# Kernel tuning notes

Hardware: AMD Instinct MI355X
Metric: run time of the kernel (lower is better)

The kernel has to match this reference:

```python
import jax, jax.numpy as jnp
import numpy as np

B, T, D = 64, 1024, 512

def setup_inputs() -> dict:
    key = jax.random.key(0)
    ks = jax.random.split(key, 5)
    s_in = 1.0 / np.sqrt(2 * D)
    s_m = 1.0 / np.sqrt(D)
    return {
        "x": jax.random.normal(ks[0], (B, T, D), dtype=jnp.float32),
        "tau_w": jax.random.normal(ks[1], (D, 2 * D), dtype=jnp.float32) * s_in,
        "tau_b": jax.random.normal(ks[2], (D,), dtype=jnp.float32) * s_in,
        "mem_w": jax.random.normal(ks[3], (D, D), dtype=jnp.float32) * s_m,
        "mem_b": jax.random.normal(ks[4], (D,), dtype=jnp.float32) * s_m,
        "threshold": jnp.asarray(0.5, dtype=jnp.float32),
    }

def reference(x, tau_w, tau_b, mem_w, mem_b, threshold):
    b, t, d = x.shape
    dt = x.dtype
    # tau_fc input is cat([xt, tau]); split weight into x-part and tau-part
    Wx = tau_w[:, :d]   # [D, D] acting on xt
    Wt = tau_w[:, d:]   # [D, D] acting on previous tau
    # precompute the parts that depend only on x (dropout=0 -> identity)
    xproj = jnp.einsum('btd,ed->bte', x, Wx) + tau_b      # tau_fc x-contribution
    m = jnp.einsum('btd,ed->bte', x, mem_w) + mem_b       # mem_fc(xt)

    def step(carry, inp):
        v, tau = carry
        xp_t, m_t = inp
        tau = jax.nn.sigmoid(xp_t + tau @ Wt.T)
        alpha = jnp.exp(-1.0 / (tau + 1e-6))
        v = alpha * v + (1.0 - alpha) * m_t
        s = (v >= threshold).astype(dt)
        v = v * (1.0 - s)
        return (v, tau), s

    v0 = jnp.zeros((b, d), dtype=dt)
    tau0 = jnp.ones((b, d), dtype=dt)
    (v, tau), spikes = jax.lax.scan(
        step, (v0, tau0),
        (jnp.swapaxes(xproj, 0, 1), jnp.swapaxes(m, 0, 1)))
    return jnp.swapaxes(spikes, 0, 1), tau, v
```

## Files before the change

kernel.cpp:

```cpp
#include <hip/hip_runtime.h>

#define BB 64
#define TT 1024
#define DD 512
#define BT (BB*TT)

#define TAUG_SLOTS (2ULL * 64 * 4 * 3 * 128)
#define SENT32 0xFFFFFFFFu

typedef float f4 __attribute__((ext_vector_type(4)));

__global__ __launch_bounds__(256, 2) void gemm_kernel(
    const float* __restrict__ x, const float* __restrict__ tau_w,
    const float* __restrict__ tau_b, const float* __restrict__ mem_w,
    const float* __restrict__ mem_b, float* __restrict__ xp, float* __restrict__ mm)
{
    __shared__ float As[32][132];
    __shared__ float Bs[32][68];

    const int tid  = threadIdx.x;
    const int bt0  = blockIdx.x * 128;
    const bool isxp = (blockIdx.y < 8);
    const float* W       = isxp ? tau_w : mem_w;
    const int    wstride = isxp ? 1024 : 512;
    const int    e0      = isxp ? blockIdx.y * 64 : blockIdx.y * 64 - 512;
    const float* bias    = isxp ? tau_b : mem_b;
    float*       dst     = isxp ? xp : mm;

    const int tm = tid & 31, tn = tid >> 5;
    const int lr = tid >> 3, lc = tid & 7;

    float bias_r[8];
#pragma unroll
    for (int ni = 0; ni < 8; ni++) bias_r[ni] = bias[e0 + tn * 8 + ni];

    float acc[4][8] = {};
    float4 pa[4], pb[2];

#pragma unroll
    for (int j = 0; j < 4; j++)
        pa[j] = *(const float4*)(x + (size_t)(bt0 + lr + 32 * j) * DD + lc * 4);
#pragma unroll
    for (int j = 0; j < 2; j++)
        pb[j] = *(const float4*)(W + (size_t)(e0 + lr + 32 * j) * wstride + lc * 4);

    for (int kb = 0; kb < DD; kb += 32) {
#pragma unroll
        for (int j = 0; j < 4; j++) {
            As[lc * 4 + 0][lr + 32 * j] = pa[j].x;
            As[lc * 4 + 1][lr + 32 * j] = pa[j].y;
            As[lc * 4 + 2][lr + 32 * j] = pa[j].z;
            As[lc * 4 + 3][lr + 32 * j] = pa[j].w;
        }
#pragma unroll
        for (int j = 0; j < 2; j++) {
            Bs[lc * 4 + 0][lr + 32 * j] = pb[j].x;
            Bs[lc * 4 + 1][lr + 32 * j] = pb[j].y;
            Bs[lc * 4 + 2][lr + 32 * j] = pb[j].z;
            Bs[lc * 4 + 3][lr + 32 * j] = pb[j].w;
        }
        __syncthreads();
        if (kb + 32 < DD) {
#pragma unroll
            for (int j = 0; j < 4; j++)
                pa[j] = *(const float4*)(x + (size_t)(bt0 + lr + 32 * j) * DD + kb + 32 + lc * 4);
#pragma unroll
            for (int j = 0; j < 2; j++)
                pb[j] = *(const float4*)(W + (size_t)(e0 + lr + 32 * j) * wstride + kb + 32 + lc * 4);
        }
#pragma unroll
        for (int k = 0; k < 32; k++) {
            float4 av  = *(const float4*)&As[k][tm * 4];
            float4 bv0 = *(const float4*)&Bs[k][tn * 8];
            float4 bv1 = *(const float4*)&Bs[k][tn * 8 + 4];
            float a_[4] = {av.x, av.y, av.z, av.w};
            float b_[8] = {bv0.x, bv0.y, bv0.z, bv0.w, bv1.x, bv1.y, bv1.z, bv1.w};
#pragma unroll
            for (int mi = 0; mi < 4; mi++)
#pragma unroll
                for (int ni = 0; ni < 8; ni++)
                    acc[mi][ni] = fmaf(a_[mi], b_[ni], acc[mi][ni]);
        }
        __syncthreads();
    }

#pragma unroll
    for (int mi = 0; mi < 4; mi++) {
        const int row = bt0 + tm * 4 + mi;
        float o[8];
#pragma unroll
        for (int ni = 0; ni < 8; ni++) o[ni] = __fadd_rn(acc[mi][ni], bias_r[ni]);
        float4 s0 = {o[0], o[1], o[2], o[3]};
        float4 s1 = {o[4], o[5], o[6], o[7]};
        *(float4*)(dst + (size_t)row * DD + e0 + tn * 8)     = s0;
        *(float4*)(dst + (size_t)row * DD + e0 + tn * 8 + 4) = s1;
    }
}

__global__ __launch_bounds__(512, 1) void scan_kernel(
    const float* __restrict__ tau_w,
    float* __restrict__ xp_sp,
    const float* __restrict__ mm,
    const float* __restrict__ thrp,
    float* __restrict__ tau_out, float* __restrict__ v_out,
    unsigned int* __restrict__ taug32)
{
    __shared__ __align__(16) float tau_buf[2][128];

    const int bid = blockIdx.x;
    const int b = bid & 63, p = bid >> 6;
    const int t = threadIdx.x;
    const int q = t >> 7;
    const int j = t & 127;
    const bool owner = (q == p);

    float wv[128];
    {
        const float4* wrow = (const float4*)(tau_w + (size_t)t * 1024 + 512 + p * 128);
#pragma unroll
        for (int jj = 0; jj < 32; jj++) {
            float4 w4 = wrow[jj];
            wv[4 * jj + 0] = w4.x; wv[4 * jj + 1] = w4.y;
            wv[4 * jj + 2] = w4.z; wv[4 * jj + 3] = w4.w;
        }
    }
#pragma unroll
    for (int jj = 0; jj < 128; jj++) asm volatile("" : "+v"(wv[jj]));

    if (t < 128) tau_buf[0][t] = 1.0f;

    const float thr = thrp[0];
    float v = 0.0f, tau_keep = 1.0f;
    const size_t baseio = (size_t)b * TT * DD + t;

    __syncthreads();

    for (int i = 0; i < TT; i++) {
        float xpv = 0.0f, mv = 0.0f;
        if (owner) {
            xpv = xp_sp[baseio + (size_t)i * DD];
            mv  = mm  [baseio + (size_t)i * DD];
        }

        float a0 = 0.f, a1 = 0.f, a2 = 0.f, a3 = 0.f;
        {
            const f4* tl = (const f4*)&tau_buf[i & 1][0];
#pragma unroll
            for (int jj = 0; jj < 32; jj++) {
                f4 t4 = tl[jj];
                a0 = fmaf(wv[4 * jj + 0], t4.x, a0);
                a1 = fmaf(wv[4 * jj + 1], t4.y, a1);
                a2 = fmaf(wv[4 * jj + 2], t4.z, a2);
                a3 = fmaf(wv[4 * jj + 3], t4.w, a3);
            }
        }
        const float part = (a0 + a1) + (a2 + a3);

        const size_t pb = (size_t)(((i & 1) * 64 + b) * 4);
        if (!owner) {
            const int cidx = (p < q) ? p : p - 1;
            __hip_atomic_store(&taug32[(pb + q) * 384 + (size_t)cidx * 128 + j],
                               __float_as_uint(part),
                               __ATOMIC_RELAXED, __HIP_MEMORY_SCOPE_AGENT);
        } else {
            unsigned int* s0 = &taug32[(pb + p) * 384 + j];
            unsigned int k0, k1, k2;
            do {
                k0 = __hip_atomic_load(s0,       __ATOMIC_RELAXED, __HIP_MEMORY_SCOPE_AGENT);
                k1 = __hip_atomic_load(s0 + 128, __ATOMIC_RELAXED, __HIP_MEMORY_SCOPE_AGENT);
                k2 = __hip_atomic_load(s0 + 256, __ATOMIC_RELAXED, __HIP_MEMORY_SCOPE_AGENT);
            } while (k0 == SENT32 || k1 == SENT32 || k2 == SENT32);
            __hip_atomic_store(s0,       SENT32, __ATOMIC_RELAXED, __HIP_MEMORY_SCOPE_AGENT);
            __hip_atomic_store(s0 + 128, SENT32, __ATOMIC_RELAXED, __HIP_MEMORY_SCOPE_AGENT);
            __hip_atomic_store(s0 + 256, SENT32, __ATOMIC_RELAXED, __HIP_MEMORY_SCOPE_AGENT);
            const float r0 = __uint_as_float(k0);
            const float r1 = __uint_as_float(k1);
            const float r2 = __uint_as_float(k2);
            const float pp0 = (p == 0) ? part : r0;
            const float pp1 = (p == 0) ? r0 : ((p == 1) ? part : r1);
            const float pp2 = (p <= 1) ? r1 : ((p == 2) ? part : r2);
            const float pp3 = (p == 3) ? part : r2;

            float dotv  = (pp0 + pp1) + (pp2 + pp3);
            float z     = __fadd_rn(xpv, dotv);
            float enz   = expf(-z);
            float tau_n = 1.0f / __fadd_rn(1.0f, enz);
            tau_keep = tau_n;
            tau_buf[(i + 1) & 1][j] = tau_n;

            float tpe   = __fadd_rn(tau_n, 1e-6f);
            float alpha = expf(-1.0f / tpe);
            float vn = __fadd_rn(__fmul_rn(alpha, v),
                                 __fmul_rn(__fsub_rn(1.0f, alpha), mv));
            bool s = (vn >= thr);
            xp_sp[baseio + (size_t)i * DD] = s ? 1.0f : 0.0f;
            v = s ? 0.0f : vn;
        }
        __syncthreads();
    }

    if (owner) {
        tau_out[b * DD + t] = tau_keep;
        v_out  [b * DD + t] = v;
    }
}

extern "C" void kernel_launch(void* const* d_in, const int* in_sizes, int n_in,
                              void* d_out, int out_size, void* d_ws, size_t ws_size,
                              hipStream_t stream) {
    (void)in_sizes; (void)n_in; (void)out_size; (void)ws_size;
    const float* x     = (const float*)d_in[0];
    const float* tau_w = (const float*)d_in[1];
    const float* tau_b = (const float*)d_in[2];
    const float* mem_w = (const float*)d_in[3];
    const float* mem_b = (const float*)d_in[4];
    const float* thr   = (const float*)d_in[5];
    float* out = (float*)d_out;

    float* mm              = (float*)d_ws;
    unsigned int* taug32   = (unsigned int*)(mm + (size_t)BT * DD);

    hipMemsetAsync(taug32, 0xFF, TAUG_SLOTS * sizeof(unsigned int), stream);

    gemm_kernel<<<dim3(512, 16), 256, 0, stream>>>(x, tau_w, tau_b, mem_w, mem_b,
                                                   out, mm);
    scan_kernel<<<256, 512, 0, stream>>>(tau_w, out, mm, thr,
                                         out + (size_t)BT * DD,
                                         out + (size_t)BT * DD + (size_t)BB * DD,
                                         taug32);
}
```

Before: 2.674 ms.

## Offload membrane update to helper wavegroup one step behind the tau critical path

```diff
diff --git a/kernel.cpp b/kernel.cpp
--- a/kernel.cpp
+++ b/kernel.cpp
@@ -112,7 +112,8 @@
     const int t = threadIdx.x;
     const int q = t >> 7;
     const int j = t & 127;
-    const bool owner = (q == p);
+    const bool owner  = (q == p);
+    const bool helper = (q == ((p + 1) & 3));
 
     float wv[128];
     {
@@ -130,17 +131,17 @@
     if (t < 128) tau_buf[0][t] = 1.0f;
 
     const float thr = thrp[0];
-    float v = 0.0f, tau_keep = 1.0f;
+    float tau_keep = 1.0f;
+    float hv = 0.0f, m_hold = 0.0f;
     const size_t baseio = (size_t)b * TT * DD + t;
+    const size_t baseH  = (size_t)b * TT * DD + p * 128 + j;
 
     __syncthreads();
 
     for (int i = 0; i < TT; i++) {
-        float xpv = 0.0f, mv = 0.0f;
-        if (owner) {
-            xpv = xp_sp[baseio + (size_t)i * DD];
-            mv  = mm  [baseio + (size_t)i * DD];
-        }
+        float xpv = 0.0f, m_next = 0.0f;
+        if (owner)  xpv    = xp_sp[baseio + (size_t)i * DD];
+        if (helper) m_next = mm   [baseH  + (size_t)i * DD];
 
         float a0 = 0.f, a1 = 0.f, a2 = 0.f, a3 = 0.f;
         {
@@ -162,7 +163,19 @@
             __hip_atomic_store(&taug32[(pb + q) * 384 + (size_t)cidx * 128 + j],
                                __float_as_uint(part),
                                __ATOMIC_RELAXED, __HIP_MEMORY_SCOPE_AGENT);
+            if (helper && i > 0) {
+                float ta    = tau_buf[i & 1][j];
+                float tpe   = __fadd_rn(ta, 1e-6f);
+                float alpha = expf(-1.0f / tpe);
+                float vn = __fadd_rn(__fmul_rn(alpha, hv),
+                                     __fmul_rn(__fsub_rn(1.0f, alpha), m_hold));
+                bool s = (vn >= thr);
+                xp_sp[baseH + (size_t)(i - 1) * DD] = s ? 1.0f : 0.0f;
+                hv = s ? 0.0f : vn;
+            }
+            if (helper) m_hold = m_next;
         } else {
+            __builtin_amdgcn_s_setprio(1);
             unsigned int* s0 = &taug32[(pb + p) * 384 + j];
             unsigned int k0, k1, k2;
             do {
@@ -187,21 +200,22 @@
             float tau_n = 1.0f / __fadd_rn(1.0f, enz);
             tau_keep = tau_n;
             tau_buf[(i + 1) & 1][j] = tau_n;
-
-            float tpe   = __fadd_rn(tau_n, 1e-6f);
-            float alpha = expf(-1.0f / tpe);
-            float vn = __fadd_rn(__fmul_rn(alpha, v),
-                                 __fmul_rn(__fsub_rn(1.0f, alpha), mv));
-            bool s = (vn >= thr);
-            xp_sp[baseio + (size_t)i * DD] = s ? 1.0f : 0.0f;
-            v = s ? 0.0f : vn;
+            __builtin_amdgcn_s_setprio(0);
         }
         __syncthreads();
     }
 
-    if (owner) {
-        tau_out[b * DD + t] = tau_keep;
-        v_out  [b * DD + t] = v;
+    if (owner) tau_out[b * DD + t] = tau_keep;
+    if (helper) {
+        float ta    = tau_buf[0][j];
+        float tpe   = __fadd_rn(ta, 1e-6f);
+        float alpha = expf(-1.0f / tpe);
+        float vn = __fadd_rn(__fmul_rn(alpha, hv),
+                             __fmul_rn(__fsub_rn(1.0f, alpha), m_hold));
+        bool s = (vn >= thr);
+        xp_sp[baseH + (size_t)(TT - 1) * DD] = s ? 1.0f : 0.0f;
+        hv = s ? 0.0f : vn;
+        v_out[b * DD + p * 128 + j] = hv;
     }
 }
 
```

Measured after the change: 2.740 ms. 2.5% more time.
